# Performance work log

Hardware: AMD Instinct MI355X
Metric: run time of the kernel (lower is better)

Reference implementation:

```python
import jax, jax.numpy as jnp
import numpy as np

B, S, E, H = 4, 1024, 1024, 16
HD = E // H


def setup_inputs() -> dict:
    key = jax.random.key(0)
    ks = jax.random.split(key, 5)
    x = jax.random.normal(ks[0], (B, S, E), dtype=jnp.float32)
    # causal mask: True = masked (filled with -inf), as in masked_fill_
    mask = jnp.triu(jnp.ones((S, S), dtype=bool), k=1)
    in_proj_weight = jax.random.normal(ks[1], (3 * E, E), dtype=jnp.float32) * (E ** -0.5)
    in_proj_bias = jax.random.normal(ks[2], (3 * E,), dtype=jnp.float32) * 0.02
    out_w = jax.random.normal(ks[3], (E, E), dtype=jnp.float32) * (E ** -0.5)
    out_b = jax.random.normal(ks[4], (E,), dtype=jnp.float32) * 0.02
    return {"x": x, "mask": mask, "in_proj_weight": in_proj_weight,
            "in_proj_bias": in_proj_bias, "out_w": out_w, "out_b": out_b}


def reference(x, mask, in_proj_weight, in_proj_bias, out_w, out_b):
    scaling = HD ** -0.5
    # fused QKV projection (self-attention path: qkv_same)
    qkv = jnp.einsum('bse,fe->bsf', x, in_proj_weight) + in_proj_bias  # [B,S,3E]
    q, k, v = jnp.split(qkv, 3, axis=-1)
    # split heads -> [B,H,S,HD]
    def heads(t):
        return t.reshape(B, S, H, HD).transpose(0, 2, 1, 3)
    q, k, v = heads(q), heads(k), heads(v)
    scores = jnp.einsum('bhsd,bhtd->bhst', q, k) * scaling  # [B,H,S,S]
    scores = jnp.where(mask[None, None, :, :], -jnp.inf, scores)
    att = jax.nn.softmax(scores, axis=-1)  # dropout p=0.0 (eval)
    out = jnp.einsum('bhst,bhtd->bhsd', att, v)  # [B,H,S,HD]
    out = out.transpose(0, 2, 1, 3).reshape(B, S, E)  # concat heads
    out = jnp.einsum('bse,fe->bsf', out, out_w) + out_b
    att_weights = att.reshape(B * H, S, S)
    return out, att_weights
```

## Files before the change

### kernel.cpp

```cpp
#include <hip/hip_runtime.h>
#include <hip/hip_bf16.h>
#include <stdint.h>

#define NH 16
#define SEQ 1024
#define EMB 1024
#define HDIM 64
#define BATCH 4
#define SPAD 1032

typedef float f32x4 __attribute__((ext_vector_type(4)));
typedef short bf16x8 __attribute__((ext_vector_type(8)));

static __device__ __forceinline__ short f2bf(float f) {
  union { float f; uint32_t u; } v; v.f = f;
  uint32_t r = (v.u + 0x7FFF + ((v.u >> 16) & 1)) >> 16;
  return (short)(uint16_t)r;
}
static __device__ __forceinline__ float bf2f(short h) {
  union { uint32_t u; float f; } v; v.u = ((uint32_t)(uint16_t)h) << 16;
  return v.f;
}

static __device__ __forceinline__ void gload_lds16(const void* g, void* l) {
  __builtin_amdgcn_global_load_lds(
      (const __attribute__((address_space(1))) void*)g,
      (__attribute__((address_space(3))) void*)l, 16, 0, 0);
}

static __device__ __forceinline__ void cvt8(const float* s, short* d) {
  const float4* sv = (const float4*)s;
  float4 a = sv[0], b = sv[1];
  bf16x8 o;
  o[0] = f2bf(a.x); o[1] = f2bf(a.y); o[2] = f2bf(a.z); o[3] = f2bf(a.w);
  o[4] = f2bf(b.x); o[5] = f2bf(b.y); o[6] = f2bf(b.z); o[7] = f2bf(b.w);
  *(bf16x8*)d = o;
}

__global__ void cvt3_kernel(const float* __restrict__ x, const float* __restrict__ w,
                            const float* __restrict__ o, short* __restrict__ xb,
                            short* __restrict__ wb, short* __restrict__ ob) {
  int i = (blockIdx.x * blockDim.x + threadIdx.x) * 8;
  if (i < 4194304) {
    cvt8(x + i, xb + i);
  } else if (i < 7340032) {
    cvt8(w + (i - 4194304), wb + (i - 4194304));
  } else {
    cvt8(o + (i - 7340032), ob + (i - 7340032));
  }
}

__global__ __launch_bounds__(256) void transpose_v(const short* __restrict__ v,
                                                   short* __restrict__ vt) {
  __shared__ short t[64][72];
  const int tid = threadIdx.x;
  const int bh = blockIdx.y;
  const int sb = blockIdx.x * 64;
  const int row = tid >> 2;
  const int c0 = (tid & 3) * 16;
  const short* src = v + ((size_t)(bh * SEQ + sb + row)) * HDIM + c0;
  *(bf16x8*)&t[row][c0] = *(const bf16x8*)src;
  *(bf16x8*)&t[row][c0 + 8] = *(const bf16x8*)(src + 8);
  __syncthreads();
  bf16x8 o0, o1;
#pragma unroll
  for (int i = 0; i < 8; ++i) o0[i] = t[c0 + i][row];
#pragma unroll
  for (int i = 0; i < 8; ++i) o1[i] = t[c0 + 8 + i][row];
  short* dst = vt + ((size_t)(bh * HDIM + row)) * SEQ + sb + c0;
  *(bf16x8*)dst = o0;
  *(bf16x8*)(dst + 8) = o1;
}

#define STAGE_QKV(bb, kk0)                                                     \
  {                                                                            \
    _Pragma("unroll") for (int c = 0; c < 4; ++c) {                            \
      int oo = o + c * 1024;                                                   \
      int row = oo >> 7;                                                       \
      int scol = (oo & 127) ^ ((row & 7) << 4);                                \
      gload_lds16((const char*)A + ((size_t)(row0 + row) * K + (kk0)) * 2 + scol, \
                  (char*)As[bb] + (w * 4 + c) * 1024);                         \
      gload_lds16((const char*)Bm + ((size_t)(col0 + row) * K + (kk0)) * 2 + scol,\
                  (char*)Bs[bb] + (w * 4 + c) * 1024);                         \
    }                                                                          \
  }

__global__ __launch_bounds__(256) void gemm_qkv(
    const short* __restrict__ A, const short* __restrict__ Bm,
    const float* __restrict__ bias, short* __restrict__ qkvws) {
  __shared__ short As[2][128 * 64];
  __shared__ short Bs[2][128 * 64];
  const int tid = threadIdx.x;
  const int w = tid >> 6, l = tid & 63;
  const int l15 = l & 15, l4 = l >> 4;
  const int wr = w >> 1, wc = w & 1;
  const int row0 = blockIdx.x * 128;
  const int col0 = blockIdx.y * 128;
  const int K = EMB;

  f32x4 acc[4][4] = {};

  const int o = (w * 4) * 1024 + l * 16;
  STAGE_QKV(0, 0);
  __syncthreads();

  int cur = 0;
  for (int k0 = 0; k0 < K; k0 += 64) {
    if (k0 + 64 < K) STAGE_QKV(cur ^ 1, k0 + 64);
#pragma unroll
    for (int kk = 0; kk < 2; ++kk) {
      bf16x8 af[4], bfr[4];
      const int kb = (kk * 64 + l4 * 16) ^ ((l15 & 7) << 4);
#pragma unroll
      for (int i = 0; i < 4; ++i) {
        af[i] = *(const bf16x8*)((const char*)As[cur] + (wr * 64 + i * 16 + l15) * 128 + kb);
        bfr[i] = *(const bf16x8*)((const char*)Bs[cur] + (wc * 64 + i * 16 + l15) * 128 + kb);
      }
#pragma unroll
      for (int i = 0; i < 4; ++i)
#pragma unroll
        for (int j = 0; j < 4; ++j)
          acc[i][j] = __builtin_amdgcn_mfma_f32_16x16x32_bf16(af[i], bfr[j], acc[i][j], 0, 0, 0);
    }
    __syncthreads();
    cur ^= 1;
  }

#pragma unroll
  for (int j = 0; j < 4; ++j) {
    int f = col0 + wc * 64 + j * 16 + l15;
    float bv = bias[f];
    int part = f >> 10;
    int e = f & 1023;
    int hh = e >> 6, d = e & 63;
#pragma unroll
    for (int i = 0; i < 4; ++i) {
#pragma unroll
      for (int rr = 0; rr < 4; ++rr) {
        int m = row0 + wr * 64 + i * 16 + l4 * 4 + rr;
        int bb = m >> 10, ss = m & 1023;
        qkvws[(size_t)part * 4194304 +
              ((size_t)(bb * NH + hh) * SEQ + ss) * HDIM + d] =
            f2bf(acc[i][j][rr] + bv);
      }
    }
  }
}

#define STAGE_OUT(bb, kk0)                                                     \
  {                                                                            \
    _Pragma("unroll") for (int c = 0; c < 4; ++c) {                            \
      int oo = oA + c * 1024;                                                  \
      int row = oo >> 7;                                                       \
      int scol = (oo & 127) ^ ((row & 7) << 4);                                \
      gload_lds16((const char*)A + ((size_t)(row0 + row) * K + (kk0)) * 2 + scol, \
                  (char*)As[bb] + (w * 4 + c) * 1024);                         \
    }                                                                          \
    _Pragma("unroll") for (int c = 0; c < 2; ++c) {                            \
      int oo = oB + c * 1024;                                                  \
      int row = oo >> 7;                                                       \
      int scol = (oo & 127) ^ ((row & 7) << 4);                                \
      gload_lds16((const char*)Bm + ((size_t)(col0 + row) * K + (kk0)) * 2 + scol,\
                  (char*)Bs[bb] + (w * 2 + c) * 1024);                         \
    }                                                                          \
  }

__global__ __launch_bounds__(256) void gemm_out64(
    const short* __restrict__ A, const short* __restrict__ Bm,
    const float* __restrict__ bias, float* __restrict__ outp) {
  __shared__ short As[2][128 * 64];
  __shared__ short Bs[2][64 * 64];
  const int tid = threadIdx.x;
  const int w = tid >> 6, l = tid & 63;
  const int l15 = l & 15, l4 = l >> 4;
  const int row0 = blockIdx.x * 128;
  const int col0 = blockIdx.y * 64;
  const int K = EMB;

  f32x4 acc[2][4] = {};

  const int oA = (w * 4) * 1024 + l * 16;
  const int oB = (w * 2) * 1024 + l * 16;
  STAGE_OUT(0, 0);
  __syncthreads();

  int cur = 0;
  for (int k0 = 0; k0 < K; k0 += 64) {
    if (k0 + 64 < K) STAGE_OUT(cur ^ 1, k0 + 64);
#pragma unroll
    for (int kk = 0; kk < 2; ++kk) {
      bf16x8 af[2], bfr[4];
      const int kb = (kk * 64 + l4 * 16) ^ ((l15 & 7) << 4);
#pragma unroll
      for (int i = 0; i < 2; ++i)
        af[i] = *(const bf16x8*)((const char*)As[cur] + (w * 32 + i * 16 + l15) * 128 + kb);
#pragma unroll
      for (int j = 0; j < 4; ++j)
        bfr[j] = *(const bf16x8*)((const char*)Bs[cur] + (j * 16 + l15) * 128 + kb);
#pragma unroll
      for (int i = 0; i < 2; ++i)
#pragma unroll
        for (int j = 0; j < 4; ++j)
          acc[i][j] = __builtin_amdgcn_mfma_f32_16x16x32_bf16(af[i], bfr[j], acc[i][j], 0, 0, 0);
    }
    __syncthreads();
    cur ^= 1;
  }

#pragma unroll
  for (int j = 0; j < 4; ++j) {
    int f = col0 + j * 16 + l15;
    float bv = bias[f];
#pragma unroll
    for (int i = 0; i < 2; ++i)
#pragma unroll
      for (int rr = 0; rr < 4; ++rr) {
        int m = row0 + w * 32 + i * 16 + l4 * 4 + rr;
        __builtin_nontemporal_store(acc[i][j][rr] + bv, &outp[(size_t)m * EMB + f]);
      }
  }
}

__global__ __launch_bounds__(256) void attn_kernel(
    const short* __restrict__ qws, const short* __restrict__ kws,
    const short* __restrict__ vtws, float* __restrict__ attg,
    short* __restrict__ aow) {
  __shared__ short strip[16 * SPAD];
  __shared__ float wsum[4][16];
  __shared__ float inv_sum[16];

  const int tid = threadIdx.x;
  const int w = tid >> 6, l = tid & 63;
  const int l15 = l & 15, l4 = l >> 4;
  const int blk = blockIdx.x;
  const int bh = blk >> 6;
  const int r = blk & 63;
  const int rowbase = r * 16;

  const short* qb = qws + ((size_t)bh * SEQ + rowbase) * HDIM;
  const short* kb = kws + (size_t)bh * SEQ * HDIM;
  const short* vb = vtws + (size_t)bh * HDIM * SEQ;

  bf16x8 qf[2];
#pragma unroll
  for (int ks = 0; ks < 2; ++ks)
    qf[ks] = *(const bf16x8*)(qb + l15 * HDIM + ks * 32 + l4 * 8);

  const int ng2 = (r + 2) & ~1;
  float psum[4] = {};

  for (int g = w; g < ng2; g += 4) {
    const short* kg = kb + (g * 16 + l15) * HDIM + l4 * 8;
    bf16x8 kf0 = *(const bf16x8*)(kg);
    bf16x8 kf1 = *(const bf16x8*)(kg + 32);
    f32x4 a0 = {};
    a0 = __builtin_amdgcn_mfma_f32_16x16x32_bf16(qf[0], kf0, a0, 0, 0, 0);
    a0 = __builtin_amdgcn_mfma_f32_16x16x32_bf16(qf[1], kf1, a0, 0, 0, 0);
    int col = g * 16 + l15;
#pragma unroll
    for (int rr = 0; rr < 4; ++rr) {
      int rloc = l4 * 4 + rr;
      int row = rowbase + rloc;
      float sv = a0[rr] * 0.125f;
      float ev = (col <= row) ? __expf(sv) : 0.0f;
      psum[rr] += ev;
      strip[rloc * SPAD + col] = f2bf(ev);
    }
  }

#pragma unroll
  for (int rr = 0; rr < 4; ++rr) {
    float v = psum[rr];
    v += __shfl_xor(v, 1);
    v += __shfl_xor(v, 2);
    v += __shfl_xor(v, 4);
    v += __shfl_xor(v, 8);
    psum[rr] = v;
  }
  if (l15 == 0) {
#pragma unroll
    for (int rr = 0; rr < 4; ++rr)
      wsum[w][l4 * 4 + rr] = psum[rr];
  }
  __syncthreads();
  if (tid < 16) {
    float s = wsum[0][tid] + wsum[1][tid] + wsum[2][tid] + wsum[3][tid];
    inv_sum[tid] = 1.0f / s;
  }
  __syncthreads();

  {
    const int limit = ng2 * 16;
    const int rloc = tid >> 4;
    const int cb = tid & 15;
    float* arow = attg + (size_t)bh * SEQ * SEQ + (size_t)(rowbase + rloc) * SEQ;
    float isr = inv_sum[rloc];
#pragma unroll
    for (int i = 0; i < 8; ++i) {
      int c = (cb + i * 16) * 8;
      f32x4 o0, o1;
      if (c < limit) {
        bf16x8 p = *(const bf16x8*)&strip[rloc * SPAD + c];
        o0[0] = bf2f(p[0]) * isr; o0[1] = bf2f(p[1]) * isr;
        o0[2] = bf2f(p[2]) * isr; o0[3] = bf2f(p[3]) * isr;
        o1[0] = bf2f(p[4]) * isr; o1[1] = bf2f(p[5]) * isr;
        o1[2] = bf2f(p[6]) * isr; o1[3] = bf2f(p[7]) * isr;
      } else {
        o0 = (f32x4)0.0f;
        o1 = (f32x4)0.0f;
      }
      __builtin_nontemporal_store(o0, (f32x4*)(arow + c));
      __builtin_nontemporal_store(o1, (f32x4*)(arow + c + 4));
    }
  }

  {
    const int nch = ng2 >> 1;
    const int d0 = w * 16;
    f32x4 oacc = {};
    const short* vrow = vb + (d0 + l15) * SEQ + l4 * 8;
    for (int c = 0; c < nch; ++c) {
      bf16x8 vf = *(const bf16x8*)(vrow + c * 32);
      bf16x8 p0 = *(const bf16x8*)&strip[l15 * SPAD + c * 32 + l4 * 8];
      oacc = __builtin_amdgcn_mfma_f32_16x16x32_bf16(p0, vf, oacc, 0, 0, 0);
    }
    const int b = bh >> 4, h = bh & 15;
#pragma unroll
    for (int rr = 0; rr < 4; ++rr) {
      int rloc = l4 * 4 + rr;
      int s = rowbase + rloc;
      float v = oacc[rr] * inv_sum[rloc];
      aow[((size_t)(b * SEQ + s)) * EMB + h * HDIM + d0 + l15] = f2bf(v);
    }
  }
}

extern "C" void kernel_launch(void* const* d_in, const int* in_sizes, int n_in,
                              void* d_out, int out_size, void* d_ws, size_t ws_size,
                              hipStream_t stream) {
  (void)in_sizes; (void)n_in; (void)out_size; (void)ws_size;
  const float* x = (const float*)d_in[0];
  const float* ipw = (const float*)d_in[2];
  const float* ipb = (const float*)d_in[3];
  const float* ow = (const float*)d_in[4];
  const float* ob = (const float*)d_in[5];
  float* outp = (float*)d_out;
  float* attg = (float*)d_out + (size_t)BATCH * SEQ * EMB;

  char* ws = (char*)d_ws;
  short* xbf = (short*)(ws);
  short* wbf = (short*)(ws + 8388608);
  short* owbf = (short*)(ws + 14680064);
  short* qkvws = (short*)(ws + 16777216);
  short* aow = (short*)(ws + 41943040);
  short* vtws = (short*)(ws);

  short* qws = qkvws;
  short* kws = qkvws + 4194304;
  short* vws = qkvws + 8388608;

  cvt3_kernel<<<4096, 256, 0, stream>>>(x, ipw, ow, xbf, wbf, owbf);

  dim3 g1(32, 24);
  gemm_qkv<<<g1, 256, 0, stream>>>(xbf, wbf, ipb, qkvws);

  transpose_v<<<dim3(16, 64), 256, 0, stream>>>(vws, vtws);

  attn_kernel<<<4096, 256, 0, stream>>>(qws, kws, vtws, attg, aow);

  gemm_out64<<<dim3(32, 16), 256, 0, stream>>>(aow, owbf, ob, outp);
}
```

Measured before the change: 183.0 us.

## Drop LDS double buffering in GEMMs and remap block order for XCD locality

Both projection GEMMs drop the two-stage LDS double buffer and go back to a single buffer: each k-step loads the tile, syncs, computes, then syncs again. This halves LDS use, which could allow more resident blocks per CU, but loads no longer overlap with MFMA work inside a block. Grids become 1-D, and block indices are remapped so that consecutive blocks landing on the same XCD (round-robin by lin&7) cover neighbouring tiles, to improve L2 reuse.

```diff
diff --git a/kernel.cpp b/kernel.cpp
--- a/kernel.cpp
+++ b/kernel.cpp
@@ -72,49 +72,45 @@
   *(bf16x8*)(dst + 8) = o1;
 }
 
-#define STAGE_QKV(bb, kk0)                                                     \
-  {                                                                            \
-    _Pragma("unroll") for (int c = 0; c < 4; ++c) {                            \
-      int oo = o + c * 1024;                                                   \
-      int row = oo >> 7;                                                       \
-      int scol = (oo & 127) ^ ((row & 7) << 4);                                \
-      gload_lds16((const char*)A + ((size_t)(row0 + row) * K + (kk0)) * 2 + scol, \
-                  (char*)As[bb] + (w * 4 + c) * 1024);                         \
-      gload_lds16((const char*)Bm + ((size_t)(col0 + row) * K + (kk0)) * 2 + scol,\
-                  (char*)Bs[bb] + (w * 4 + c) * 1024);                         \
-    }                                                                          \
-  }
-
 __global__ __launch_bounds__(256) void gemm_qkv(
     const short* __restrict__ A, const short* __restrict__ Bm,
     const float* __restrict__ bias, short* __restrict__ qkvws) {
-  __shared__ short As[2][128 * 64];
-  __shared__ short Bs[2][128 * 64];
+  __shared__ short As[128 * 64];
+  __shared__ short Bs[128 * 64];
   const int tid = threadIdx.x;
   const int w = tid >> 6, l = tid & 63;
   const int l15 = l & 15, l4 = l >> 4;
   const int wr = w >> 1, wc = w & 1;
-  const int row0 = blockIdx.x * 128;
-  const int col0 = blockIdx.y * 128;
+  const int lin = blockIdx.x;
+  const int gid = (lin & 7) * 96 + (lin >> 3);
+  const int row0 = (gid & 31) * 128;
+  const int col0 = (gid >> 5) * 128;
   const int K = EMB;
 
   f32x4 acc[4][4] = {};
 
   const int o = (w * 4) * 1024 + l * 16;
-  STAGE_QKV(0, 0);
-  __syncthreads();
-
-  int cur = 0;
   for (int k0 = 0; k0 < K; k0 += 64) {
-    if (k0 + 64 < K) STAGE_QKV(cur ^ 1, k0 + 64);
+#pragma unroll
+    for (int c = 0; c < 4; ++c) {
+      int oo = o + c * 1024;
+      int row = oo >> 7;
+      int colb = oo & 127;
+      int scol = colb ^ ((row & 7) << 4);
+      gload_lds16((const char*)A + ((size_t)(row0 + row) * K + k0) * 2 + scol,
+                  (char*)As + (w * 4 + c) * 1024);
+      gload_lds16((const char*)Bm + ((size_t)(col0 + row) * K + k0) * 2 + scol,
+                  (char*)Bs + (w * 4 + c) * 1024);
+    }
+    __syncthreads();
 #pragma unroll
     for (int kk = 0; kk < 2; ++kk) {
       bf16x8 af[4], bfr[4];
       const int kb = (kk * 64 + l4 * 16) ^ ((l15 & 7) << 4);
 #pragma unroll
       for (int i = 0; i < 4; ++i) {
-        af[i] = *(const bf16x8*)((const char*)As[cur] + (wr * 64 + i * 16 + l15) * 128 + kb);
-        bfr[i] = *(const bf16x8*)((const char*)Bs[cur] + (wc * 64 + i * 16 + l15) * 128 + kb);
+        af[i] = *(const bf16x8*)((const char*)As + (wr * 64 + i * 16 + l15) * 128 + kb);
+        bfr[i] = *(const bf16x8*)((const char*)Bs + (wc * 64 + i * 16 + l15) * 128 + kb);
       }
 #pragma unroll
       for (int i = 0; i < 4; ++i)
@@ -123,7 +119,6 @@
           acc[i][j] = __builtin_amdgcn_mfma_f32_16x16x32_bf16(af[i], bfr[j], acc[i][j], 0, 0, 0);
     }
     __syncthreads();
-    cur ^= 1;
   }
 
 #pragma unroll
@@ -147,56 +142,54 @@
   }
 }
 
-#define STAGE_OUT(bb, kk0)                                                     \
-  {                                                                            \
-    _Pragma("unroll") for (int c = 0; c < 4; ++c) {                            \
-      int oo = oA + c * 1024;                                                  \
-      int row = oo >> 7;                                                       \
-      int scol = (oo & 127) ^ ((row & 7) << 4);                                \
-      gload_lds16((const char*)A + ((size_t)(row0 + row) * K + (kk0)) * 2 + scol, \
-                  (char*)As[bb] + (w * 4 + c) * 1024);                         \
-    }                                                                          \
-    _Pragma("unroll") for (int c = 0; c < 2; ++c) {                            \
-      int oo = oB + c * 1024;                                                  \
-      int row = oo >> 7;                                                       \
-      int scol = (oo & 127) ^ ((row & 7) << 4);                                \
-      gload_lds16((const char*)Bm + ((size_t)(col0 + row) * K + (kk0)) * 2 + scol,\
-                  (char*)Bs[bb] + (w * 2 + c) * 1024);                         \
-    }                                                                          \
-  }
-
 __global__ __launch_bounds__(256) void gemm_out64(
     const short* __restrict__ A, const short* __restrict__ Bm,
     const float* __restrict__ bias, float* __restrict__ outp) {
-  __shared__ short As[2][128 * 64];
-  __shared__ short Bs[2][64 * 64];
+  __shared__ short As[128 * 64];
+  __shared__ short Bs[64 * 64];
   const int tid = threadIdx.x;
   const int w = tid >> 6, l = tid & 63;
   const int l15 = l & 15, l4 = l >> 4;
-  const int row0 = blockIdx.x * 128;
-  const int col0 = blockIdx.y * 64;
+  const int lin = blockIdx.x;
+  const int gid = (lin & 7) * 64 + (lin >> 3);
+  const int row0 = (gid & 31) * 128;
+  const int col0 = (gid >> 5) * 64;
   const int K = EMB;
 
   f32x4 acc[2][4] = {};
 
   const int oA = (w * 4) * 1024 + l * 16;
   const int oB = (w * 2) * 1024 + l * 16;
-  STAGE_OUT(0, 0);
-  __syncthreads();
-
-  int cur = 0;
   for (int k0 = 0; k0 < K; k0 += 64) {
-    if (k0 + 64 < K) STAGE_OUT(cur ^ 1, k0 + 64);
+#pragma unroll
+    for (int c = 0; c < 4; ++c) {
+      int oo = oA + c * 1024;
+      int row = oo >> 7;
+      int colb = oo & 127;
+      int scol = colb ^ ((row & 7) << 4);
+      gload_lds16((const char*)A + ((size_t)(row0 + row) * K + k0) * 2 + scol,
+                  (char*)As + (w * 4 + c) * 1024);
+    }
+#pragma unroll
+    for (int c = 0; c < 2; ++c) {
+      int oo = oB + c * 1024;
+      int row = oo >> 7;
+      int colb = oo & 127;
+      int scol = colb ^ ((row & 7) << 4);
+      gload_lds16((const char*)Bm + ((size_t)(col0 + row) * K + k0) * 2 + scol,
+                  (char*)Bs + (w * 2 + c) * 1024);
+    }
+    __syncthreads();
 #pragma unroll
     for (int kk = 0; kk < 2; ++kk) {
       bf16x8 af[2], bfr[4];
       const int kb = (kk * 64 + l4 * 16) ^ ((l15 & 7) << 4);
 #pragma unroll
       for (int i = 0; i < 2; ++i)
-        af[i] = *(const bf16x8*)((const char*)As[cur] + (w * 32 + i * 16 + l15) * 128 + kb);
+        af[i] = *(const bf16x8*)((const char*)As + (w * 32 + i * 16 + l15) * 128 + kb);
 #pragma unroll
       for (int j = 0; j < 4; ++j)
-        bfr[j] = *(const bf16x8*)((const char*)Bs[cur] + (j * 16 + l15) * 128 + kb);
+        bfr[j] = *(const bf16x8*)((const char*)Bs + (j * 16 + l15) * 128 + kb);
 #pragma unroll
       for (int i = 0; i < 2; ++i)
 #pragma unroll
@@ -204,7 +197,6 @@
           acc[i][j] = __builtin_amdgcn_mfma_f32_16x16x32_bf16(af[i], bfr[j], acc[i][j], 0, 0, 0);
     }
     __syncthreads();
-    cur ^= 1;
   }
 
 #pragma unroll
@@ -361,12 +353,11 @@
 
   cvt3_kernel<<<4096, 256, 0, stream>>>(x, ipw, ow, xbf, wbf, owbf);
 
-  dim3 g1(32, 24);
-  gemm_qkv<<<g1, 256, 0, stream>>>(xbf, wbf, ipb, qkvws);
+  gemm_qkv<<<768, 256, 0, stream>>>(xbf, wbf, ipb, qkvws);
 
   transpose_v<<<dim3(16, 64), 256, 0, stream>>>(vws, vtws);
 
   attn_kernel<<<4096, 256, 0, stream>>>(qws, kws, vtws, attg, aow);
 
-  gemm_out64<<<dim3(32, 16), 256, 0, stream>>>(aow, owbf, ob, outp);
-}
+  gemm_out64<<<512, 256, 0, stream>>>(aow, owbf, ob, outp);
+}
```

New measurement: 195.9 us. 1.07x slower.
